# Kernel tuning notes

Measured on AMD Instinct MI355X. Metric: run time of the kernel, lower is better.

Reference implementation:

```python
import jax, jax.numpy as jnp
import numpy as np

B, S, D = 2, 2048, 1024
H, DK = 16, 64  # num_heads, key_dim (value_dim defaults to key_dim)


def setup_inputs() -> dict:
    key = jax.random.key(0)
    ks = jax.random.split(key, 11)
    init = lambda k, shape, fan_in: jax.random.uniform(
        k, shape, jnp.float32, -1.0, 1.0) * (1.0 / np.sqrt(fan_in))
    return {
        "query": jax.random.normal(ks[0], (B, S, D), jnp.float32),
        "key": jax.random.normal(ks[1], (B, S, D), jnp.float32),
        "value": jax.random.normal(ks[2], (B, S, D), jnp.float32),
        "Wq": init(ks[3], (D, H, DK), D),
        "bq": jnp.zeros((H, DK), jnp.float32),
        "Wk": init(ks[4], (D, H, DK), D),
        "bk": jnp.zeros((H, DK), jnp.float32),
        "Wv": init(ks[5], (D, H, DK), D),
        "bv": jnp.zeros((H, DK), jnp.float32),
        "Wo": init(ks[6], (H, DK, D), H * DK),
        "bo": jnp.zeros((D,), jnp.float32),
    }


def reference(query, key, value, Wq, bq, Wk, bk, Wv, bv, Wo, bo):
    # QKV projections: abc,cde->abde (EinsumDense with bias on (H, DK))
    q = jnp.einsum("bsd,dhk->bshk", query, Wq) + bq  # [B,S,H,DK]
    k = jnp.einsum("bsd,dhk->bshk", key, Wk) + bk
    v = jnp.einsum("bsd,dhk->bshk", value, Wv) + bv
    # Keras scales the query before the dot product
    q = q * (1.0 / jnp.sqrt(jnp.asarray(DK, q.dtype)))
    # aecd,abcd->acbe : [B,H,Sq,Sk]
    scores = jnp.einsum("bqhk,bshk->bhqs", q, k)
    probs = jax.nn.softmax(scores, axis=-1)
    # acbe,aecd->abcd : [B,Sq,H,DK]
    attn = jnp.einsum("bhqs,bshk->bqhk", probs, v)
    # output projection: abcd,cde->abe
    out = jnp.einsum("bqhk,hkd->bqd", attn, Wo) + bo  # [B,S,D]
    return out
```

## Files before the change

### kernel.cpp

```cpp
#include <hip/hip_runtime.h>
#include <hip/hip_bf16.h>
#include <stdint.h>
#include <stddef.h>


typedef __bf16 bf16;
typedef __attribute__((ext_vector_type(4))) bf16 bf16x4;
typedef __attribute__((ext_vector_type(8))) bf16 bf16x8;
typedef __attribute__((ext_vector_type(4))) float f32x4;
typedef __attribute__((ext_vector_type(16))) float f32x16;
typedef __attribute__((ext_vector_type(2))) unsigned int uint2v;

#define DEVINL static __device__ __forceinline__

DEVINL void gload_lds16(const void* g, void* l) {
  __builtin_amdgcn_global_load_lds(
      (const __attribute__((address_space(1))) void*)g,
      (__attribute__((address_space(3))) void*)l, 16, 0, 0);
}

DEVINL f32x4 mfma16(bf16x8 a, bf16x8 b, f32x4 c) {
  return __builtin_amdgcn_mfma_f32_16x16x32_bf16(a, b, c, 0, 0, 0);
}
DEVINL f32x16 mfma32(bf16x8 a, bf16x8 b, f32x16 c) {
  return __builtin_amdgcn_mfma_f32_32x32x16_bf16(a, b, c, 0, 0, 0);
}
DEVINL float fexp2(float x) {
  float r;
  asm("v_exp_f32 %0, %1" : "=v"(r) : "v"(x));
  return r;
}
DEVINL unsigned pack2(float lo, float hi) {
  union { bf16 h[2]; unsigned u; } t;
  t.h[0] = (bf16)lo; t.h[1] = (bf16)hi;
  return t.u;
}
DEVINL bf16x8 mk8(unsigned a, unsigned b, unsigned c, unsigned d) {
  union { unsigned u[4]; bf16x8 v; } t;
  t.u[0] = a; t.u[1] = b; t.u[2] = c; t.u[3] = d;
  return t.v;
}

__global__ __launch_bounds__(256) void prep_kernel(
    const float* __restrict__ q, const float* __restrict__ k,
    const float* __restrict__ v,
    const float* __restrict__ w0, const float* __restrict__ w1,
    const float* __restrict__ w2, const float* __restrict__ w3,
    bf16* __restrict__ Abf, bf16* __restrict__ Wt) {
  __shared__ float tile[64 * 65];
  int bx = blockIdx.x;
  if (bx < 6144) {
    int z = bx >> 11, blk = bx & 2047;
    const float* src = (z == 0) ? q : (z == 1) ? k : v;
    size_t off = ((size_t)blk * 256 + threadIdx.x) * 8;
    f32x4 a = *(const f32x4*)(src + off);
    f32x4 b = *(const f32x4*)(src + off + 4);
    bf16x8 h;
#pragma unroll
    for (int j = 0; j < 4; ++j) { h[j] = (bf16)a[j]; h[4 + j] = (bf16)b[j]; }
    *(bf16x8*)(Abf + (size_t)z * 4194304 + off) = h;
  } else {
    int tb = bx - 6144;
    int t = tb >> 8;
    tb &= 255;
    const float* w = (t == 0) ? w0 : (t == 1) ? w1 : (t == 2) ? w2 : w3;
    bf16* o = Wt + (size_t)t * 1024 * 1024;
    int k0 = (tb >> 4) * 64, n0 = (tb & 15) * 64;
    int c = threadIdx.x & 63, r0 = threadIdx.x >> 6;
    for (int r = r0; r < 64; r += 4)
      tile[r * 65 + c] = w[(size_t)(k0 + r) * 1024 + n0 + c];
    __syncthreads();
    for (int r = r0; r < 64; r += 4)
      o[(size_t)(n0 + r) * 1024 + k0 + c] = (bf16)tile[c * 65 + r];
  }
}

__global__ __launch_bounds__(256) void gemm_qkv(
    const bf16* __restrict__ Abf, const bf16* __restrict__ Wt,
    const float* __restrict__ bq, const float* __restrict__ bk,
    const float* __restrict__ bv,
    bf16* __restrict__ outQ, bf16* __restrict__ outK, bf16* __restrict__ Vt) {
  int z = blockIdx.z;
  const bf16* A    = Abf + (size_t)z * 4194304;
  const bf16* Wz   = Wt + (size_t)z * 1024 * 1024;
  const float* bia = (z == 0) ? bq : (z == 1) ? bk : bv;
  float scale      = (z == 0) ? 0.18033688011112042f : 1.0f;

  __shared__ bf16 As[2][128 * 32];
  __shared__ bf16 Bs[2][128 * 32];

  int m0 = blockIdx.x * 128, n0 = blockIdx.y * 128;
  int tid = threadIdx.x, w = tid >> 6, l = tid & 63;
  int wm = (w >> 1) * 64, wn = (w & 1) * 64;
  int c16 = l & 15, g = l >> 4;
  int rsw = (c16 >> 1) & 3;

  int brow0 = (w * 2 + 0) * 16 + (l >> 2);
  int brow1 = (w * 2 + 1) * 16 + (l >> 2);
  int bk0 = ((l & 3) ^ ((brow0 >> 1) & 3)) * 8;
  int bk1 = ((l & 3) ^ ((brow1 >> 1) & 3)) * 8;

  f32x4 acc[4][4] = {};

#define STAGE_QKV(buf, kt)                                                   \
  do {                                                                       \
    gload_lds16(A + (size_t)(m0 + brow0) * 1024 + (kt) + bk0,                \
                (char*)As[buf] + (w * 2 + 0) * 1024 + l * 16);               \
    gload_lds16(A + (size_t)(m0 + brow1) * 1024 + (kt) + bk1,                \
                (char*)As[buf] + (w * 2 + 1) * 1024 + l * 16);               \
    gload_lds16(Wz + (size_t)(n0 + brow0) * 1024 + (kt) + bk0,               \
                (char*)Bs[buf] + (w * 2 + 0) * 1024 + l * 16);               \
    gload_lds16(Wz + (size_t)(n0 + brow1) * 1024 + (kt) + bk1,               \
                (char*)Bs[buf] + (w * 2 + 1) * 1024 + l * 16);               \
  } while (0)

  STAGE_QKV(0, 0);
  __syncthreads();

  int cur = 0;
  for (int kt = 0; kt < 1024; kt += 32) {
    if (kt < 992) STAGE_QKV(cur ^ 1, kt + 32);
    bf16x8 af[4], bfr[4];
#pragma unroll
    for (int mt = 0; mt < 4; ++mt)
      af[mt] = *(const bf16x8*)&As[cur][(wm + mt * 16 + c16) * 32 + ((g ^ rsw) * 8)];
#pragma unroll
    for (int nt = 0; nt < 4; ++nt)
      bfr[nt] = *(const bf16x8*)&Bs[cur][(wn + nt * 16 + c16) * 32 + ((g ^ rsw) * 8)];
#pragma unroll
    for (int mt = 0; mt < 4; ++mt)
#pragma unroll
      for (int nt = 0; nt < 4; ++nt)
        acc[mt][nt] = mfma16(af[mt], bfr[nt], acc[mt][nt]);
    __syncthreads();
    cur ^= 1;
  }
#undef STAGE_QKV

  if (z < 2) {
    bf16* Cout = (z == 0) ? outQ : outK;
#pragma unroll
    for (int mt = 0; mt < 4; ++mt)
#pragma unroll
      for (int nt = 0; nt < 4; ++nt) {
        int n = n0 + wn + nt * 16 + c16;
        float bb = bia[n];
#pragma unroll
        for (int r = 0; r < 4; ++r) {
          int m = m0 + wm + mt * 16 + g * 4 + r;
          Cout[(size_t)m * 1024 + n] = (bf16)((acc[mt][nt][r] + bb) * scale);
        }
      }
  } else {
#pragma unroll
    for (int mt = 0; mt < 4; ++mt)
#pragma unroll
      for (int nt = 0; nt < 4; ++nt) {
        int n = n0 + wn + nt * 16 + c16;
        float bb = bia[n];
        int m = m0 + wm + mt * 16 + g * 4;
        int b = m >> 11, s = m & 2047;
        bf16x4 v;
#pragma unroll
        for (int r = 0; r < 4; ++r) v[r] = (bf16)(acc[mt][nt][r] + bb);
        *(bf16x4*)&Vt[((size_t)(b * 16 + (n >> 6)) * 64 + (n & 63)) * 2048 + s] = v;
      }
  }
}

__global__ __launch_bounds__(256) void flash_kernel(
    const bf16* __restrict__ Qp, const bf16* __restrict__ Kp,
    const bf16* __restrict__ Vt, bf16* __restrict__ AO) {
  __shared__ __align__(16) bf16 Ks[4][64 * 64];
  __shared__ __align__(16) bf16 Vs[4][64 * 64];

  int orig = blockIdx.x;
  int wg = (orig & 7) * 64 + (orig >> 3);
  int bh = wg >> 4, qb = wg & 15;
  int b = bh >> 4, h = bh & 15;
  int tid = threadIdx.x, w = tid >> 6, l = tid & 63;
  int lo5 = l & 31, g = l >> 5;
  int q0 = qb * 128 + w * 32;

  const bf16* qptr = Qp + (size_t)(b * 2048 + q0 + lo5) * 1024 + h * 64 + g * 8;
  bf16x8 qf0 = *(const bf16x8*)(qptr + 0);
  bf16x8 qf1 = *(const bf16x8*)(qptr + 16);
  bf16x8 qf2 = *(const bf16x8*)(qptr + 32);
  bf16x8 qf3 = *(const bf16x8*)(qptr + 48);

  const bf16* kbase = Kp + (size_t)(b * 2048) * 1024 + h * 64;
  const bf16* vbase = Vt + (size_t)bh * 64 * 2048;

  int u0 = w * 64 + l;
  int u1 = (4 + w) * 64 + l;
  int r0s = u0 >> 3, c0s = (u0 & 7) ^ (r0s & 7);
  int r1s = u1 >> 3, c1s = (u1 & 7) ^ (r1s & 7);

#define STAGE(buf, s0)                                                          \
  do {                                                                          \
    gload_lds16(kbase + (size_t)((s0) + r0s) * 1024 + c0s * 8,                  \
                (bf16*)Ks[buf] + u0 * 8);                                       \
    gload_lds16(kbase + (size_t)((s0) + r1s) * 1024 + c1s * 8,                  \
                (bf16*)Ks[buf] + u1 * 8);                                       \
    gload_lds16(vbase + (size_t)r0s * 2048 + (s0) + c0s * 8,                    \
                (bf16*)Vs[buf] + u0 * 8);                                       \
    gload_lds16(vbase + (size_t)r1s * 2048 + (s0) + c1s * 8,                    \
                (bf16*)Vs[buf] + u1 * 8);                                       \
  } while (0)

#define LDSK(cp, nt, kt) \
  (*(const bf16x8*)&cp[(((nt)*32 + lo5) << 6) + (((((kt)*2 + g)) ^ (lo5 & 7)) << 3)])
#define LDSV(cp, dt, st) \
  (*(const bf16x8*)&cp[(((dt)*32 + lo5) << 6) + (((((st)*2 + g)) ^ (lo5 & 7)) << 3)])

  f32x16 o0 = {}, o1 = {};
  float ps0 = 0.f, ps1 = 0.f, ps2 = 0.f, ps3 = 0.f;

  STAGE(0, 0);
  STAGE(1, 64);
  for (int t = 0; t < 32; ++t) {
    if (t < 30) {
      STAGE((t + 2) & 3, (t + 2) * 64);
      asm volatile("s_waitcnt vmcnt(8)" ::: "memory");
    } else if (t == 30) {
      asm volatile("s_waitcnt vmcnt(4)" ::: "memory");
    } else {
      asm volatile("s_waitcnt vmcnt(0)" ::: "memory");
    }
    __builtin_amdgcn_s_barrier();
    __builtin_amdgcn_sched_barrier(0);
    const bf16* kc = Ks[t & 3];
    const bf16* vc = Vs[t & 3];

    f32x16 sv = {};
    __builtin_amdgcn_s_setprio(1);
    sv = mfma32(LDSK(kc, 0, 0), qf0, sv);
    sv = mfma32(LDSK(kc, 0, 1), qf1, sv);
    sv = mfma32(LDSK(kc, 0, 2), qf2, sv);
    sv = mfma32(LDSK(kc, 0, 3), qf3, sv);
    __builtin_amdgcn_s_setprio(0);
    float p[16];
#pragma unroll
    for (int r = 0; r < 16; ++r) p[r] = fexp2(sv[r]);
    ps0 += p[0] + p[4] + p[8] + p[12];
    ps1 += p[1] + p[5] + p[9] + p[13];
    ps2 += p[2] + p[6] + p[10] + p[14];
    ps3 += p[3] + p[7] + p[11] + p[15];
    unsigned pw0 = pack2(p[0], p[1]), pw1 = pack2(p[2], p[3]);
    unsigned pw2 = pack2(p[4], p[5]), pw3 = pack2(p[6], p[7]);
    unsigned pw4 = pack2(p[8], p[9]), pw5 = pack2(p[10], p[11]);
    unsigned pw6 = pack2(p[12], p[13]), pw7 = pack2(p[14], p[15]);
    uint2v a02 = __builtin_amdgcn_permlane32_swap(pw0, pw2, false, false);
    uint2v a13 = __builtin_amdgcn_permlane32_swap(pw1, pw3, false, false);
    uint2v a46 = __builtin_amdgcn_permlane32_swap(pw4, pw6, false, false);
    uint2v a57 = __builtin_amdgcn_permlane32_swap(pw5, pw7, false, false);
    bf16x8 pa0 = mk8(a02.x, a13.x, a02.y, a13.y);
    bf16x8 pa1 = mk8(a46.x, a57.x, a46.y, a57.y);

    f32x16 sw = {};
    __builtin_amdgcn_s_setprio(1);
    sw = mfma32(LDSK(kc, 1, 0), qf0, sw);
    sw = mfma32(LDSK(kc, 1, 1), qf1, sw);
    sw = mfma32(LDSK(kc, 1, 2), qf2, sw);
    sw = mfma32(LDSK(kc, 1, 3), qf3, sw);
    __builtin_amdgcn_s_setprio(0);
#pragma unroll
    for (int r = 0; r < 16; ++r) p[r] = fexp2(sw[r]);
    ps0 += p[0] + p[4] + p[8] + p[12];
    ps1 += p[1] + p[5] + p[9] + p[13];
    ps2 += p[2] + p[6] + p[10] + p[14];
    ps3 += p[3] + p[7] + p[11] + p[15];
    pw0 = pack2(p[0], p[1]); pw1 = pack2(p[2], p[3]);
    pw2 = pack2(p[4], p[5]); pw3 = pack2(p[6], p[7]);
    pw4 = pack2(p[8], p[9]); pw5 = pack2(p[10], p[11]);
    pw6 = pack2(p[12], p[13]); pw7 = pack2(p[14], p[15]);
    a02 = __builtin_amdgcn_permlane32_swap(pw0, pw2, false, false);
    a13 = __builtin_amdgcn_permlane32_swap(pw1, pw3, false, false);
    a46 = __builtin_amdgcn_permlane32_swap(pw4, pw6, false, false);
    a57 = __builtin_amdgcn_permlane32_swap(pw5, pw7, false, false);
    bf16x8 pb0 = mk8(a02.x, a13.x, a02.y, a13.y);
    bf16x8 pb1 = mk8(a46.x, a57.x, a46.y, a57.y);

    __builtin_amdgcn_s_setprio(1);
    o0 = mfma32(pa0, LDSV(vc, 0, 0), o0);
    o1 = mfma32(pa0, LDSV(vc, 1, 0), o1);
    o0 = mfma32(pa1, LDSV(vc, 0, 1), o0);
    o1 = mfma32(pa1, LDSV(vc, 1, 1), o1);
    o0 = mfma32(pb0, LDSV(vc, 0, 2), o0);
    o1 = mfma32(pb0, LDSV(vc, 1, 2), o1);
    o0 = mfma32(pb1, LDSV(vc, 0, 3), o0);
    o1 = mfma32(pb1, LDSV(vc, 1, 3), o1);
    __builtin_amdgcn_s_setprio(0);
  }
#undef STAGE
#undef LDSK
#undef LDSV

  float plsum = (ps0 + ps1) + (ps2 + ps3);
  float tot = plsum + __shfl_xor(plsum, 32);

#pragma unroll
  for (int r = 0; r < 16; ++r) {
    int qr = (r & 3) + 8 * (r >> 2) + 4 * g;
    float inv = 1.0f / __shfl(tot, qr);
    bf16* op = AO + (size_t)(b * 2048 + q0 + qr) * 1024 + h * 64 + lo5;
    op[0]  = (bf16)(o0[r] * inv);
    op[32] = (bf16)(o1[r] * inv);
  }
}

__global__ __launch_bounds__(256) void gemm_o(
    const bf16* __restrict__ A, const bf16* __restrict__ Wt3,
    const float* __restrict__ bo, float* __restrict__ C) {
  __shared__ bf16 As[2][64 * 32];
  __shared__ bf16 Bs[2][128 * 32];
  int m0 = blockIdx.x * 64, n0 = blockIdx.y * 128;
  int tid = threadIdx.x, w = tid >> 6, l = tid & 63;
  int wm = (w >> 1) * 32, wn = (w & 1) * 64;
  int c16 = l & 15, g = l >> 4;
  int rsw = (c16 >> 1) & 3;

  int arow = tid >> 2, akc = tid & 3;
  int asrc = (akc ^ ((arow >> 1) & 3)) * 8;
  int brow0 = (w * 2 + 0) * 16 + (l >> 2);
  int brow1 = (w * 2 + 1) * 16 + (l >> 2);
  int bk0 = ((l & 3) ^ ((brow0 >> 1) & 3)) * 8;
  int bk1 = ((l & 3) ^ ((brow1 >> 1) & 3)) * 8;

  f32x4 acc[2][4] = {};

#define STAGE_O(buf, kt)                                                     \
  do {                                                                       \
    gload_lds16(A + (size_t)(m0 + arow) * 1024 + (kt) + asrc,                \
                (char*)As[buf] + tid * 16);                                  \
    gload_lds16(Wt3 + (size_t)(n0 + brow0) * 1024 + (kt) + bk0,              \
                (char*)Bs[buf] + (w * 2 + 0) * 1024 + l * 16);               \
    gload_lds16(Wt3 + (size_t)(n0 + brow1) * 1024 + (kt) + bk1,              \
                (char*)Bs[buf] + (w * 2 + 1) * 1024 + l * 16);               \
  } while (0)

  STAGE_O(0, 0);
  __syncthreads();

  int cur = 0;
  for (int kt = 0; kt < 1024; kt += 32) {
    if (kt < 992) STAGE_O(cur ^ 1, kt + 32);
    bf16x8 af[2], bfr[4];
#pragma unroll
    for (int mt = 0; mt < 2; ++mt)
      af[mt] = *(const bf16x8*)&As[cur][(wm + mt * 16 + c16) * 32 + ((g ^ rsw) * 8)];
#pragma unroll
    for (int nt = 0; nt < 4; ++nt)
      bfr[nt] = *(const bf16x8*)&Bs[cur][(wn + nt * 16 + c16) * 32 + ((g ^ rsw) * 8)];
#pragma unroll
    for (int mt = 0; mt < 2; ++mt)
#pragma unroll
      for (int nt = 0; nt < 4; ++nt)
        acc[mt][nt] = mfma16(af[mt], bfr[nt], acc[mt][nt]);
    __syncthreads();
    cur ^= 1;
  }
#undef STAGE_O

#pragma unroll
  for (int mt = 0; mt < 2; ++mt)
#pragma unroll
    for (int nt = 0; nt < 4; ++nt) {
      int n = n0 + wn + nt * 16 + c16;
      float bb = bo[n];
#pragma unroll
      for (int r = 0; r < 4; ++r) {
        int m = m0 + wm + mt * 16 + g * 4 + r;
        C[(size_t)m * 1024 + n] = acc[mt][nt][r] + bb;
      }
    }
}

extern "C" void kernel_launch(void* const* d_in, const int* in_sizes, int n_in,
                              void* d_out, int out_size, void* d_ws, size_t ws_size,
                              hipStream_t stream) {
  const float* query = (const float*)d_in[0];
  const float* key_  = (const float*)d_in[1];
  const float* value = (const float*)d_in[2];
  const float* Wq = (const float*)d_in[3];
  const float* bq = (const float*)d_in[4];
  const float* Wk = (const float*)d_in[5];
  const float* bk = (const float*)d_in[6];
  const float* Wv = (const float*)d_in[7];
  const float* bv = (const float*)d_in[8];
  const float* Wo = (const float*)d_in[9];
  const float* bo = (const float*)d_in[10];
  float* out = (float*)d_out;

  char* ws = (char*)d_ws;
  const size_t MB = 1024 * 1024;
  bf16* Wt  = (bf16*)(ws);
  bf16* Abf = (bf16*)(ws + 8 * MB);
  bf16* Qp  = (bf16*)(ws + 32 * MB);
  bf16* Kp  = (bf16*)(ws + 40 * MB);
  bf16* Vt  = (bf16*)(ws + 48 * MB);
  bf16* AO  = (bf16*)(ws + 8 * MB);

  dim3 blk(256);
  prep_kernel<<<dim3(7168), blk, 0, stream>>>(query, key_, value,
                                              Wq, Wk, Wv, Wo, Abf, Wt);
  gemm_qkv<<<dim3(32, 8, 3), blk, 0, stream>>>(Abf, Wt, bq, bk, bv, Qp, Kp, Vt);
  flash_kernel<<<dim3(512), blk, 0, stream>>>(Qp, Kp, Vt, AO);
  gemm_o<<<dim3(64, 8), blk, 0, stream>>>(AO, Wt + (size_t)3 * 1024 * 1024, bo, out);
}
```

Before: 132.8 us.

## Fuse fp32-to-bf16 input conversion into QKV GEMM and batch flash QK MFMAs

Removes the separate activation conversion pass: the QKV GEMM now loads fp32 activations straight into LDS with an XOR swizzle and converts them to bf16 when building MFMA fragments. This drops one full read and write of the three 2x2048x1024 inputs, but doubles the A-tile LDS footprint and global load traffic inside the GEMM and adds conversion ALU work per k-step. The flash kernel also issues both QK^T MFMA groups back to back before the exponentials, and a sched_barrier is added at the end of each loop iteration.

```diff
diff --git a/kernel.cpp b/kernel.cpp
--- a/kernel.cpp
+++ b/kernel.cpp
@@ -41,53 +41,38 @@
   return t.v;
 }
 
-__global__ __launch_bounds__(256) void prep_kernel(
-    const float* __restrict__ q, const float* __restrict__ k,
-    const float* __restrict__ v,
+__global__ __launch_bounds__(256) void wt_kernel(
     const float* __restrict__ w0, const float* __restrict__ w1,
     const float* __restrict__ w2, const float* __restrict__ w3,
-    bf16* __restrict__ Abf, bf16* __restrict__ Wt) {
+    bf16* __restrict__ out) {
   __shared__ float tile[64 * 65];
-  int bx = blockIdx.x;
-  if (bx < 6144) {
-    int z = bx >> 11, blk = bx & 2047;
-    const float* src = (z == 0) ? q : (z == 1) ? k : v;
-    size_t off = ((size_t)blk * 256 + threadIdx.x) * 8;
-    f32x4 a = *(const f32x4*)(src + off);
-    f32x4 b = *(const f32x4*)(src + off + 4);
-    bf16x8 h;
-#pragma unroll
-    for (int j = 0; j < 4; ++j) { h[j] = (bf16)a[j]; h[4 + j] = (bf16)b[j]; }
-    *(bf16x8*)(Abf + (size_t)z * 4194304 + off) = h;
-  } else {
-    int tb = bx - 6144;
-    int t = tb >> 8;
-    tb &= 255;
-    const float* w = (t == 0) ? w0 : (t == 1) ? w1 : (t == 2) ? w2 : w3;
-    bf16* o = Wt + (size_t)t * 1024 * 1024;
-    int k0 = (tb >> 4) * 64, n0 = (tb & 15) * 64;
-    int c = threadIdx.x & 63, r0 = threadIdx.x >> 6;
-    for (int r = r0; r < 64; r += 4)
-      tile[r * 65 + c] = w[(size_t)(k0 + r) * 1024 + n0 + c];
-    __syncthreads();
-    for (int r = r0; r < 64; r += 4)
-      o[(size_t)(n0 + r) * 1024 + k0 + c] = (bf16)tile[c * 65 + r];
-  }
+  int t = blockIdx.y;
+  const float* w = (t == 0) ? w0 : (t == 1) ? w1 : (t == 2) ? w2 : w3;
+  bf16* o = out + (size_t)t * 1024 * 1024;
+  int tb = blockIdx.x;
+  int k0 = (tb >> 4) * 64, n0 = (tb & 15) * 64;
+  int c = threadIdx.x & 63, r0 = threadIdx.x >> 6;
+  for (int r = r0; r < 64; r += 4)
+    tile[r * 65 + c] = w[(size_t)(k0 + r) * 1024 + n0 + c];
+  __syncthreads();
+  for (int r = r0; r < 64; r += 4)
+    o[(size_t)(n0 + r) * 1024 + k0 + c] = (bf16)tile[c * 65 + r];
 }
 
 __global__ __launch_bounds__(256) void gemm_qkv(
-    const bf16* __restrict__ Abf, const bf16* __restrict__ Wt,
+    const float* __restrict__ Aq, const float* __restrict__ Ak,
+    const float* __restrict__ Av, const bf16* __restrict__ Wt,
     const float* __restrict__ bq, const float* __restrict__ bk,
     const float* __restrict__ bv,
     bf16* __restrict__ outQ, bf16* __restrict__ outK, bf16* __restrict__ Vt) {
   int z = blockIdx.z;
-  const bf16* A    = Abf + (size_t)z * 4194304;
+  const float* A   = (z == 0) ? Aq : (z == 1) ? Ak : Av;
   const bf16* Wz   = Wt + (size_t)z * 1024 * 1024;
   const float* bia = (z == 0) ? bq : (z == 1) ? bk : bv;
   float scale      = (z == 0) ? 0.18033688011112042f : 1.0f;
 
-  __shared__ bf16 As[2][128 * 32];
-  __shared__ bf16 Bs[2][128 * 32];
+  __shared__ float Af[2][128 * 32];
+  __shared__ bf16  Bs[2][128 * 32];
 
   int m0 = blockIdx.x * 128, n0 = blockIdx.y * 128;
   int tid = threadIdx.x, w = tid >> 6, l = tid & 63;
@@ -95,6 +80,13 @@
   int c16 = l & 15, g = l >> 4;
   int rsw = (c16 >> 1) & 3;
 
+  int ua[4], arow[4], asrc[4];
+#pragma unroll
+  for (int i = 0; i < 4; ++i) {
+    ua[i] = (w * 4 + i) * 64 + l;
+    arow[i] = ua[i] >> 3;
+    asrc[i] = ((ua[i] & 7) ^ (arow[i] & 7)) * 4;
+  }
   int brow0 = (w * 2 + 0) * 16 + (l >> 2);
   int brow1 = (w * 2 + 1) * 16 + (l >> 2);
   int bk0 = ((l & 3) ^ ((brow0 >> 1) & 3)) * 8;
@@ -104,10 +96,9 @@
 
 #define STAGE_QKV(buf, kt)                                                   \
   do {                                                                       \
-    gload_lds16(A + (size_t)(m0 + brow0) * 1024 + (kt) + bk0,                \
-                (char*)As[buf] + (w * 2 + 0) * 1024 + l * 16);               \
-    gload_lds16(A + (size_t)(m0 + brow1) * 1024 + (kt) + bk1,                \
-                (char*)As[buf] + (w * 2 + 1) * 1024 + l * 16);               \
+    _Pragma("unroll") for (int i = 0; i < 4; ++i)                            \
+      gload_lds16(A + (size_t)(m0 + arow[i]) * 1024 + (kt) + asrc[i],        \
+                  (char*)Af[buf] + ua[i] * 16);                              \
     gload_lds16(Wz + (size_t)(n0 + brow0) * 1024 + (kt) + bk0,               \
                 (char*)Bs[buf] + (w * 2 + 0) * 1024 + l * 16);               \
     gload_lds16(Wz + (size_t)(n0 + brow1) * 1024 + (kt) + bk1,               \
@@ -122,8 +113,16 @@
     if (kt < 992) STAGE_QKV(cur ^ 1, kt + 32);
     bf16x8 af[4], bfr[4];
 #pragma unroll
-    for (int mt = 0; mt < 4; ++mt)
-      af[mt] = *(const bf16x8*)&As[cur][(wm + mt * 16 + c16) * 32 + ((g ^ rsw) * 8)];
+    for (int mt = 0; mt < 4; ++mt) {
+      int row = wm + mt * 16 + c16;
+      int r7 = row & 7;
+      f32x4 lo = *(const f32x4*)&Af[cur][row * 32 + (((2 * g)     ^ r7) << 2)];
+      f32x4 hi = *(const f32x4*)&Af[cur][row * 32 + (((2 * g + 1) ^ r7) << 2)];
+      bf16x8 h;
+#pragma unroll
+      for (int j = 0; j < 4; ++j) { h[j] = (bf16)lo[j]; h[4 + j] = (bf16)hi[j]; }
+      af[mt] = h;
+    }
 #pragma unroll
     for (int nt = 0; nt < 4; ++nt)
       bfr[nt] = *(const bf16x8*)&Bs[cur][(wn + nt * 16 + c16) * 32 + ((g ^ rsw) * 8)];
@@ -232,13 +231,18 @@
     const bf16* kc = Ks[t & 3];
     const bf16* vc = Vs[t & 3];
 
-    f32x16 sv = {};
+    f32x16 sv = {}, sw = {};
     __builtin_amdgcn_s_setprio(1);
     sv = mfma32(LDSK(kc, 0, 0), qf0, sv);
     sv = mfma32(LDSK(kc, 0, 1), qf1, sv);
     sv = mfma32(LDSK(kc, 0, 2), qf2, sv);
     sv = mfma32(LDSK(kc, 0, 3), qf3, sv);
+    sw = mfma32(LDSK(kc, 1, 0), qf0, sw);
+    sw = mfma32(LDSK(kc, 1, 1), qf1, sw);
+    sw = mfma32(LDSK(kc, 1, 2), qf2, sw);
+    sw = mfma32(LDSK(kc, 1, 3), qf3, sw);
     __builtin_amdgcn_s_setprio(0);
+
     float p[16];
 #pragma unroll
     for (int r = 0; r < 16; ++r) p[r] = fexp2(sv[r]);
@@ -257,13 +261,6 @@
     bf16x8 pa0 = mk8(a02.x, a13.x, a02.y, a13.y);
     bf16x8 pa1 = mk8(a46.x, a57.x, a46.y, a57.y);
 
-    f32x16 sw = {};
-    __builtin_amdgcn_s_setprio(1);
-    sw = mfma32(LDSK(kc, 1, 0), qf0, sw);
-    sw = mfma32(LDSK(kc, 1, 1), qf1, sw);
-    sw = mfma32(LDSK(kc, 1, 2), qf2, sw);
-    sw = mfma32(LDSK(kc, 1, 3), qf3, sw);
-    __builtin_amdgcn_s_setprio(0);
 #pragma unroll
     for (int r = 0; r < 16; ++r) p[r] = fexp2(sw[r]);
     ps0 += p[0] + p[4] + p[8] + p[12];
@@ -291,6 +288,7 @@
     o0 = mfma32(pb1, LDSV(vc, 0, 3), o0);
     o1 = mfma32(pb1, LDSV(vc, 1, 3), o1);
     __builtin_amdgcn_s_setprio(0);
+    __builtin_amdgcn_sched_barrier(0);
   }
 #undef STAGE
 #undef LDSK
@@ -395,16 +393,15 @@
   char* ws = (char*)d_ws;
   const size_t MB = 1024 * 1024;
   bf16* Wt  = (bf16*)(ws);
-  bf16* Abf = (bf16*)(ws + 8 * MB);
-  bf16* Qp  = (bf16*)(ws + 32 * MB);
-  bf16* Kp  = (bf16*)(ws + 40 * MB);
-  bf16* Vt  = (bf16*)(ws + 48 * MB);
-  bf16* AO  = (bf16*)(ws + 8 * MB);
+  bf16* Qp  = (bf16*)(ws + 8 * MB);
+  bf16* Kp  = (bf16*)(ws + 16 * MB);
+  bf16* Vt  = (bf16*)(ws + 24 * MB);
+  bf16* AO  = (bf16*)(ws + 32 * MB);
 
   dim3 blk(256);
-  prep_kernel<<<dim3(7168), blk, 0, stream>>>(query, key_, value,
-                                              Wq, Wk, Wv, Wo, Abf, Wt);
-  gemm_qkv<<<dim3(32, 8, 3), blk, 0, stream>>>(Abf, Wt, bq, bk, bv, Qp, Kp, Vt);
+  wt_kernel<<<dim3(256, 4), blk, 0, stream>>>(Wq, Wk, Wv, Wo, Wt);
+  gemm_qkv<<<dim3(32, 8, 3), blk, 0, stream>>>(query, key_, value, Wt,
+                                               bq, bk, bv, Qp, Kp, Vt);
   flash_kernel<<<dim3(512), blk, 0, stream>>>(Qp, Kp, Vt, AO);
   gemm_o<<<dim3(64, 8), blk, 0, stream>>>(AO, Wt + (size_t)3 * 1024 * 1024, bo, out);
 }
```

Result: no change. 131.9 us (-0.7%).
